# Kernel optimization log

Measured on AMD Instinct MI355X. Metric: run time of the kernel, lower is better.

The kernel has to match this reference:

```python
import jax, jax.numpy as jnp
import numpy as np

CROSS_SIZES = [256, 256, 256]  # split_half=True -> carried field sizes [39,128,128,256]


def setup_inputs() -> dict:
    key = jax.random.key(0)
    ks = jax.random.split(key, 6)
    B, F, D = 1024, 39, 32
    scale = 0.05
    return {
        "x": jax.random.normal(ks[0], (B, F, D), dtype=jnp.float32),
        "W0": jax.random.normal(ks[1], (F * F, 256), dtype=jnp.float32) * scale,
        "b0": jnp.zeros((256,), dtype=jnp.float32),
        "W1": jax.random.normal(ks[2], (F * 128, 256), dtype=jnp.float32) * scale,
        "b1": jnp.zeros((256,), dtype=jnp.float32),
        "W2": jax.random.normal(ks[3], (F * 128, 256), dtype=jnp.float32) * scale,
        "b2": jnp.zeros((256,), dtype=jnp.float32),
        "fc_w": jax.random.normal(ks[4], (512, 1), dtype=jnp.float32) * scale,
        "fc_b": jnp.zeros((1,), dtype=jnp.float32),
    }


def reference(x, W0, b0, W1, b1, W2, b2, fc_w, fc_b):
    # x: (B, F, D)
    B, F, D = x.shape
    params = [(W0, b0), (W1, b1), (W2, b2)]
    n_layers = len(params)
    x0 = x
    h = x            # carried state, (B, Hi, D)
    finals = []
    for i, (W, b) in enumerate(params):
        Hp = h.shape[1]
        # per-embedding-dim outer product of fields, flattened: (B, D, F*Hp)
        z = jnp.einsum('bfd,bhd->bdfh', x0, h).reshape(B, D, F * Hp)
        # conv1d with kernel width 1 == dense projection over the F*Hp axis
        out = jax.nn.relu(z @ W + b)          # (B, D, O)
        out = jnp.transpose(out, (0, 2, 1))   # (B, O, D)
        if i != n_layers - 1:
            half = CROSS_SIZES[i] // 2
            h = out[:, :half]        # next_tmp (first half)
            finals.append(out[:, half:])  # h (second half)
        else:
            finals.append(out)
    res = jnp.concatenate(finals, axis=1)  # (B, 512, D)
    res = jnp.sum(res, axis=-1)            # (B, 512)
    return res @ fc_w + fc_b               # (B, 1)
```

## Files before the change

kernel.cpp:

```cpp
#include <hip/hip_runtime.h>
#include <stdint.h>


typedef unsigned int u32;
typedef unsigned short u16;
typedef __attribute__((ext_vector_type(8))) unsigned short us8;
typedef __attribute__((ext_vector_type(8))) _Float16 half8;
typedef __attribute__((ext_vector_type(4))) float f32x4;

__device__ __forceinline__ u16 f32_to_f16u(float f) {
  union { _Float16 h; u16 u; } c;
  c.h = (_Float16)f;
  return c.u;
}
__device__ __forceinline__ u32 pkmul(u32 a, u32 b) {
  u32 r;
  asm("v_pk_mul_f16 %0, %1, %2" : "=v"(r) : "v"(a), "v"(b));
  return r;
}
__device__ __forceinline__ void gload16(const u16* g, u16* l) {
  __builtin_amdgcn_global_load_lds((const __attribute__((address_space(1))) u32*)g,
                                   (__attribute__((address_space(3))) u32*)l, 16, 0, 0);
}

__global__ void prep_wt(const float* __restrict__ W0, const float* __restrict__ W1,
                        const float* __restrict__ W2, u16* __restrict__ WT0,
                        u16* __restrict__ WT1, u16* __restrict__ WT2) {
  int blk = blockIdx.x;
  const float* W;
  u16* WT;
  int KPAD, kp0;
  bool l0 = false;
  if (blk < 312) { W = W0; WT = WT0; KPAD = 2496; kp0 = blk * 8; l0 = true; }
  else if (blk < 936) { W = W1; WT = WT1; KPAD = 4992; kp0 = (blk - 312) * 8; }
  else { W = W2; WT = WT2; KPAD = 4992; kp0 = (blk - 936) * 8; }

  __shared__ u16 lds[8][257];
  int t = threadIdx.x;
  #pragma unroll
  for (int kk = 0; kk < 8; ++kk) {
    int kp = kp0 + kk;
    float v;
    if (l0) {
      int f = kp >> 6, hh = kp & 63;
      v = (hh < 39) ? W[(f * 39 + hh) * 256 + t] : 0.f;
    } else {
      v = W[kp * 256 + t];
    }
    lds[kk][t] = f32_to_f16u(v);
  }
  __syncthreads();
  us8 o;
  #pragma unroll
  for (int kk = 0; kk < 8; ++kk) o[kk] = lds[kk][t];
  *(us8*)(&WT[(size_t)t * KPAD + kp0]) = o;
}

template <int LAYER>
__global__ __launch_bounds__(512, 2) void cin_layer(
    const float* __restrict__ x, const u16* __restrict__ hin,
    const u16* __restrict__ WT, const float* __restrict__ bias,
    u16* __restrict__ hout, float* __restrict__ fsum) {
  constexpr int HPAD = (LAYER == 0) ? 64 : 128;
  constexpr int HROW = HPAD + 8;
  constexpr int KPAD = 39 * HPAD;
  constexpr int HC2 = HPAD / 64;
  constexpr int NT = 39 * HC2;

  __shared__ __align__(16) u16 wtile[2][256 * 64];
  __shared__ __align__(16) u16 hT[4][32][HROW];
  __shared__ u32 x0pk[4][32][41];

  const int tid = threadIdx.x;
  const int bbase = blockIdx.x * 4;

  for (int idx = tid; idx < 4 * 1248; idx += 512) {
    int b = idx / 1248;
    int rem = idx - b * 1248;
    int f = rem >> 5, d = rem & 31;
    u16 xh = f32_to_f16u(x[(bbase + b) * 1248 + rem]);
    x0pk[b][d][f] = (u32)xh | ((u32)xh << 16);
    if (LAYER == 0) hT[b][d][f] = xh;
  }
  if (LAYER == 0) {
    for (int idx = tid; idx < 4 * 32 * 25; idx += 512) {
      int b = idx / 800;
      int rem = idx - b * 800;
      int d = rem / 25, p = rem - d * 25;
      hT[b][d][39 + p] = 0;
    }
  } else {
    for (int idx = tid; idx < 4 * 32 * 16; idx += 512) {
      int b = idx >> 9, rem = idx & 511;
      int d = rem >> 4, c = rem & 15;
      us8 v = *(const us8*)(&hin[(((bbase + b) * 32 + d) << 7) + c * 8]);
      *(us8*)(&hT[b][d][c * 8]) = v;
    }
  }

  const int lane = tid & 63;
  const int w = tid >> 6;
  const int l15 = lane & 15;
  const int g = lane >> 4;

  const int nloc = lane >> 3, slot = lane & 7;
  const int qq = slot ^ nloc;
  const int cp = qq >> 2, kcp = qq & 3;
  const u16* wsrc = WT + (size_t)(w * 32 + nloc) * KPAD + cp * 32 + kcp * 8;

  const int xorm = (l15 & 7) * 8;
  const int rB0 = (w * 32 + l15) * 64;

  f32x4 acc[8][2];
  #pragma unroll
  for (int m = 0; m < 8; ++m)
    #pragma unroll
    for (int n = 0; n < 2; ++n) acc[m][n] = (f32x4){0.f, 0.f, 0.f, 0.f};

  {
    u16* dst = &wtile[0][(w * 32) * 64];
    #pragma unroll
    for (int j = 0; j < 4; ++j) gload16(wsrc + (size_t)j * 8 * KPAD, dst + j * 8 * 64);
  }
  __syncthreads();

  union HF { u32 u[4]; half8 h; us8 s; };
  int tt = 0;
  for (int t = 0; t < HC2; ++t) {
    HF hf2[8][2];
    #pragma unroll
    for (int m = 0; m < 8; ++m)
      #pragma unroll
      for (int c = 0; c < 2; ++c)
        hf2[m][c].s = *(const us8*)(&hT[m >> 1][(m & 1) * 16 + l15][(2 * t + c) * 32 + g * 8]);
    for (int f = 0; f < 39; ++f, ++tt) {
      const int buf = tt & 1;
      if (tt + 1 < NT) {
        const int nf = (f + 1 < 39) ? f + 1 : 0;
        const int ntp = (f + 1 < 39) ? t : t + 1;
        const int koff = nf * HPAD + ntp * 64;
        u16* dst = &wtile[buf ^ 1][(w * 32) * 64];
        #pragma unroll
        for (int j = 0; j < 4; ++j)
          gload16(wsrc + (size_t)j * 8 * KPAD + koff, dst + j * 8 * 64);
      }
      u32 xs[8];
      #pragma unroll
      for (int m = 0; m < 8; ++m) xs[m] = x0pk[m >> 1][(m & 1) * 16 + l15][f];
      #pragma unroll
      for (int c = 0; c < 2; ++c) {
        const int off = (c * 32 + g * 8) ^ xorm;
        HF b0, b1;
        b0.s = *(const us8*)(&wtile[buf][rB0 + off]);
        b1.s = *(const us8*)(&wtile[buf][rB0 + 16 * 64 + off]);
        #pragma unroll
        for (int m = 0; m < 8; ++m) {
          HF a;
          #pragma unroll
          for (int i = 0; i < 4; ++i) a.u[i] = pkmul(hf2[m][c].u[i], xs[m]);
          acc[m][0] = __builtin_amdgcn_mfma_f32_16x16x32_f16(a.h, b0.h, acc[m][0], 0, 0, 0);
          acc[m][1] = __builtin_amdgcn_mfma_f32_16x16x32_f16(a.h, b1.h, acc[m][1], 0, 0, 0);
        }
      }
      __syncthreads();
    }
  }

  float bv[2];
  #pragma unroll
  for (int nt = 0; nt < 2; ++nt) bv[nt] = bias[w * 32 + nt * 16 + l15];

  if (LAYER < 2 && w < 4) {
    #pragma unroll
    for (int m = 0; m < 8; ++m)
      #pragma unroll
      for (int nt = 0; nt < 2; ++nt) {
        int o = w * 32 + nt * 16 + l15;
        #pragma unroll
        for (int r = 0; r < 4; ++r) {
          int row = m * 16 + g * 4 + r;
          int s = row >> 5, d = row & 31;
          float v = fmaxf(acc[m][nt][r] + bv[nt], 0.f);
          hout[(((bbase + s) * 32 + d) << 7) + o] = f32_to_f16u(v);
        }
      }
  } else {
    #pragma unroll
    for (int nt = 0; nt < 2; ++nt) {
      float sub[4] = {0.f, 0.f, 0.f, 0.f};
      #pragma unroll
      for (int m = 0; m < 8; ++m)
        #pragma unroll
        for (int r = 0; r < 4; ++r)
          sub[m >> 1] += fmaxf(acc[m][nt][r] + bv[nt], 0.f);
      #pragma unroll
      for (int s = 0; s < 4; ++s) {
        sub[s] += __shfl_xor(sub[s], 16);
        sub[s] += __shfl_xor(sub[s], 32);
      }
      if (lane < 16) {
        int o = w * 32 + nt * 16 + l15;
        int j = (LAYER == 0) ? (o - 128) : ((LAYER == 1) ? o : (256 + o));
        #pragma unroll
        for (int s = 0; s < 4; ++s) fsum[(bbase + s) * 512 + j] = sub[s];
      }
    }
  }
}

__global__ void finalize(const float* __restrict__ fsum, const float* __restrict__ fc_w,
                         const float* __restrict__ fc_b, float* __restrict__ out) {
  int b = blockIdx.x;
  int lane = threadIdx.x;
  const float* fs = fsum + (size_t)b * 512;
  float s = 0.f;
  #pragma unroll
  for (int k = 0; k < 8; ++k) {
    int j = k * 64 + lane;
    s += fs[j] * fc_w[j];
  }
  #pragma unroll
  for (int off = 32; off; off >>= 1) s += __shfl_xor(s, off);
  if (lane == 0) out[b] = s + fc_b[0];
}

extern "C" void kernel_launch(void* const* d_in, const int* in_sizes, int n_in,
                              void* d_out, int out_size, void* d_ws, size_t ws_size,
                              hipStream_t stream) {
  const float* x = (const float*)d_in[0];
  const float* W0 = (const float*)d_in[1];
  const float* b0 = (const float*)d_in[2];
  const float* W1 = (const float*)d_in[3];
  const float* b1 = (const float*)d_in[4];
  const float* W2 = (const float*)d_in[5];
  const float* b2 = (const float*)d_in[6];
  const float* fc_w = (const float*)d_in[7];
  const float* fc_b = (const float*)d_in[8];
  float* out = (float*)d_out;

  char* ws = (char*)d_ws;
  size_t oWT0 = 0;
  size_t oWT1 = oWT0 + (size_t)256 * 2496 * 2;
  size_t oWT2 = oWT1 + (size_t)256 * 4992 * 2;
  size_t oH = oWT2 + (size_t)256 * 4992 * 2;
  size_t oFS = oH + (size_t)1024 * 32 * 128 * 2;
  u16* WT0 = (u16*)(ws + oWT0);
  u16* WT1 = (u16*)(ws + oWT1);
  u16* WT2 = (u16*)(ws + oWT2);
  u16* hbuf = (u16*)(ws + oH);
  float* fsum = (float*)(ws + oFS);

  prep_wt<<<1560, 256, 0, stream>>>(W0, W1, W2, WT0, WT1, WT2);
  cin_layer<0><<<256, 512, 0, stream>>>(x, nullptr, WT0, b0, hbuf, fsum);
  cin_layer<1><<<256, 512, 0, stream>>>(x, hbuf, WT1, b1, hbuf, fsum);
  cin_layer<2><<<256, 512, 0, stream>>>(x, hbuf, WT2, b2, nullptr, fsum);
  finalize<<<1024, 64, 0, stream>>>(fsum, fc_w, fc_b, out);
}
```

Before: 235.7 us.

## Restructure CIN main loop with register prefetch and precomputed fp16 x0 layout

Adds a prep kernel that converts x0 into an fp16 layout ordered per d-lane/field, so each lane fetches its eight x0 scalars with one 16-byte global load instead of reading packed duplicates from LDS. Uses op_sel on v_pk_mul_f16 to broadcast the low or high half, which removes the duplicated packed x0 LDS array. The main loop is flattened and unrolled in pairs. Weight fragments for the next tile are read into registers after an explicit vmcnt wait instead of a per-tile __syncthreads. This is meant to cut LDS traffic and barrier stalls, but removing the block barrier while double-buffering through LDS risks races between waves, and the loop now carries more registers.

After: 196.8 us. -16.5%, faster.

```diff
diff --git a/kernel.cpp b/kernel.cpp
--- a/kernel.cpp
+++ b/kernel.cpp
@@ -13,14 +13,23 @@
   c.h = (_Float16)f;
   return c.u;
 }
-__device__ __forceinline__ u32 pkmul(u32 a, u32 b) {
+__device__ __forceinline__ u32 pkmul_blo(u32 a, u32 b) {
   u32 r;
-  asm("v_pk_mul_f16 %0, %1, %2" : "=v"(r) : "v"(a), "v"(b));
+  asm("v_pk_mul_f16 %0, %1, %2 op_sel:[0,0] op_sel_hi:[1,0]" : "=v"(r) : "v"(a), "v"(b));
+  return r;
+}
+__device__ __forceinline__ u32 pkmul_bhi(u32 a, u32 b) {
+  u32 r;
+  asm("v_pk_mul_f16 %0, %1, %2 op_sel:[0,1] op_sel_hi:[1,1]" : "=v"(r) : "v"(a), "v"(b));
   return r;
 }
 __device__ __forceinline__ void gload16(const u16* g, u16* l) {
   __builtin_amdgcn_global_load_lds((const __attribute__((address_space(1))) u32*)g,
                                    (__attribute__((address_space(3))) u32*)l, 16, 0, 0);
+}
+__device__ __forceinline__ void wait_vm0_sb() {
+  asm volatile("s_waitcnt vmcnt(0)" ::: "memory");
+  __builtin_amdgcn_sched_barrier(0);
 }
 
 __global__ void prep_wt(const float* __restrict__ W0, const float* __restrict__ W1,
@@ -56,11 +65,24 @@
   *(us8*)(&WT[(size_t)t * KPAD + kp0]) = o;
 }
 
+__global__ void prep_xg(const float* __restrict__ x, u16* __restrict__ xg) {
+  int bb = blockIdx.x;
+  int t = threadIdx.x;
+  for (int idx = t; idx < 4992; idx += 256) {
+    int dl = idx / 312;
+    int rem = idx - dl * 312;
+    int f = rem >> 3, m = rem & 7;
+    float v = x[(size_t)(bb * 4 + (m >> 1)) * 1248 + f * 32 + (m & 1) * 16 + dl];
+    xg[(size_t)bb * 4992 + idx] = f32_to_f16u(v);
+  }
+}
+
 template <int LAYER>
 __global__ __launch_bounds__(512, 2) void cin_layer(
     const float* __restrict__ x, const u16* __restrict__ hin,
-    const u16* __restrict__ WT, const float* __restrict__ bias,
-    u16* __restrict__ hout, float* __restrict__ fsum) {
+    const u16* __restrict__ WT, const u16* __restrict__ xg,
+    const float* __restrict__ bias, u16* __restrict__ hout,
+    float* __restrict__ fsum) {
   constexpr int HPAD = (LAYER == 0) ? 64 : 128;
   constexpr int HROW = HPAD + 8;
   constexpr int KPAD = 39 * HPAD;
@@ -69,20 +91,17 @@
 
   __shared__ __align__(16) u16 wtile[2][256 * 64];
   __shared__ __align__(16) u16 hT[4][32][HROW];
-  __shared__ u32 x0pk[4][32][41];
 
   const int tid = threadIdx.x;
   const int bbase = blockIdx.x * 4;
 
-  for (int idx = tid; idx < 4 * 1248; idx += 512) {
-    int b = idx / 1248;
-    int rem = idx - b * 1248;
-    int f = rem >> 5, d = rem & 31;
-    u16 xh = f32_to_f16u(x[(bbase + b) * 1248 + rem]);
-    x0pk[b][d][f] = (u32)xh | ((u32)xh << 16);
-    if (LAYER == 0) hT[b][d][f] = xh;
-  }
   if (LAYER == 0) {
+    for (int idx = tid; idx < 4 * 1248; idx += 512) {
+      int b = idx / 1248;
+      int rem = idx - b * 1248;
+      int f = rem >> 5, d = rem & 31;
+      hT[b][d][f] = f32_to_f16u(x[(bbase + b) * 1248 + rem]);
+    }
     for (int idx = tid; idx < 4 * 32 * 25; idx += 512) {
       int b = idx / 800;
       int rem = idx - b * 800;
@@ -105,11 +124,11 @@
 
   const int nloc = lane >> 3, slot = lane & 7;
   const int qq = slot ^ nloc;
-  const int cp = qq >> 2, kcp = qq & 3;
-  const u16* wsrc = WT + (size_t)(w * 32 + nloc) * KPAD + cp * 32 + kcp * 8;
+  const u16* wsrc = WT + (size_t)(w * 32 + nloc) * KPAD + qq * 8;
 
   const int xorm = (l15 & 7) * 8;
   const int rB0 = (w * 32 + l15) * 64;
+  const u16* xrow = xg + (size_t)blockIdx.x * 4992 + l15 * 312;
 
   f32x4 acc[8][2];
   #pragma unroll
@@ -125,46 +144,85 @@
   __syncthreads();
 
   union HF { u32 u[4]; half8 h; us8 s; };
-  int tt = 0;
-  for (int t = 0; t < HC2; ++t) {
-    HF hf2[8][2];
-    #pragma unroll
-    for (int m = 0; m < 8; ++m)
-      #pragma unroll
-      for (int c = 0; c < 2; ++c)
-        hf2[m][c].s = *(const us8*)(&hT[m >> 1][(m & 1) * 16 + l15][(2 * t + c) * 32 + g * 8]);
-    for (int f = 0; f < 39; ++f, ++tt) {
-      const int buf = tt & 1;
-      if (tt + 1 < NT) {
-        const int nf = (f + 1 < 39) ? f + 1 : 0;
-        const int ntp = (f + 1 < 39) ? t : t + 1;
-        const int koff = nf * HPAD + ntp * 64;
-        u16* dst = &wtile[buf ^ 1][(w * 32) * 64];
-        #pragma unroll
-        for (int j = 0; j < 4; ++j)
-          gload16(wsrc + (size_t)j * 8 * KPAD + koff, dst + j * 8 * 64);
-      }
-      u32 xs[8];
-      #pragma unroll
-      for (int m = 0; m < 8; ++m) xs[m] = x0pk[m >> 1][(m & 1) * 16 + l15][f];
-      #pragma unroll
-      for (int c = 0; c < 2; ++c) {
-        const int off = (c * 32 + g * 8) ^ xorm;
-        HF b0, b1;
-        b0.s = *(const us8*)(&wtile[buf][rB0 + off]);
-        b1.s = *(const us8*)(&wtile[buf][rB0 + 16 * 64 + off]);
-        #pragma unroll
-        for (int m = 0; m < 8; ++m) {
-          HF a;
-          #pragma unroll
-          for (int i = 0; i < 4; ++i) a.u[i] = pkmul(hf2[m][c].u[i], xs[m]);
-          acc[m][0] = __builtin_amdgcn_mfma_f32_16x16x32_f16(a.h, b0.h, acc[m][0], 0, 0, 0);
-          acc[m][1] = __builtin_amdgcn_mfma_f32_16x16x32_f16(a.h, b1.h, acc[m][1], 0, 0, 0);
-        }
-      }
-      __syncthreads();
-    }
-  }
+  union XQ { u32 u[4]; us8 s; };
+
+  HF hf2[8][2];
+  #pragma unroll
+  for (int m = 0; m < 8; ++m)
+    #pragma unroll
+    for (int c = 0; c < 2; ++c)
+      hf2[m][c].s = *(const us8*)(&hT[m >> 1][(m & 1) * 16 + l15][c * 32 + g * 8]);
+
+  HF fr[2][2];
+  XQ xqA, xqB;
+  #pragma unroll
+  for (int c = 0; c < 2; ++c) {
+    const int off = (c * 32 + g * 8) ^ xorm;
+    fr[c][0].s = *(const us8*)(&wtile[0][rB0 + off]);
+    fr[c][1].s = *(const us8*)(&wtile[0][rB0 + 16 * 64 + off]);
+  }
+  xqA.s = *(const us8*)(xrow);
+
+  int f = 0, hc = 0, tt = 0;
+
+#define TILE_BODY(XC, XN)                                                          \
+  {                                                                                \
+    const int buf = tt & 1;                                                        \
+    const bool more = (tt + 1 < NT);                                               \
+    int nf = f + 1, nhc = hc;                                                      \
+    if (nf == 39) { nf = 0; ++nhc; }                                               \
+    if (more) {                                                                    \
+      const int koff = nf * HPAD + nhc * 64;                                       \
+      u16* dst = &wtile[buf ^ 1][(w * 32) * 64];                                   \
+      _Pragma("unroll")                                                            \
+      for (int j = 0; j < 4; ++j)                                                  \
+        gload16(wsrc + (size_t)j * 8 * KPAD + koff, dst + j * 8 * 64);             \
+      XN.s = *(const us8*)(xrow + nf * 8);                                         \
+      __builtin_amdgcn_sched_barrier(0);                                           \
+    }                                                                              \
+    _Pragma("unroll")                                                              \
+    for (int c = 0; c < 2; ++c) {                                                  \
+      _Pragma("unroll")                                                            \
+      for (int m = 0; m < 8; ++m) {                                                \
+        HF a;                                                                      \
+        _Pragma("unroll")                                                          \
+        for (int i = 0; i < 4; ++i)                                                \
+          a.u[i] = (m & 1) ? pkmul_bhi(hf2[m][c].u[i], XC.u[m >> 1])               \
+                           : pkmul_blo(hf2[m][c].u[i], XC.u[m >> 1]);              \
+        acc[m][0] = __builtin_amdgcn_mfma_f32_16x16x32_f16(a.h, fr[c][0].h,        \
+                                                           acc[m][0], 0, 0, 0);    \
+        acc[m][1] = __builtin_amdgcn_mfma_f32_16x16x32_f16(a.h, fr[c][1].h,        \
+                                                           acc[m][1], 0, 0, 0);    \
+      }                                                                            \
+    }                                                                              \
+    if (more) {                                                                    \
+      wait_vm0_sb();                                                               \
+      _Pragma("unroll")                                                            \
+      for (int c = 0; c < 2; ++c) {                                                \
+        const int off = (c * 32 + g * 8) ^ xorm;                                   \
+        fr[c][0].s = *(const us8*)(&wtile[buf ^ 1][rB0 + off]);                    \
+        fr[c][1].s = *(const us8*)(&wtile[buf ^ 1][rB0 + 16 * 64 + off]);          \
+      }                                                                            \
+      if (nhc != hc) {                                                             \
+        _Pragma("unroll")                                                          \
+        for (int m = 0; m < 8; ++m)                                                \
+          _Pragma("unroll")                                                        \
+          for (int c = 0; c < 2; ++c)                                              \
+            hf2[m][c].s = *(const us8*)(                                           \
+                &hT[m >> 1][(m & 1) * 16 + l15][(2 * nhc + c) * 32 + g * 8]);      \
+      }                                                                            \
+    }                                                                              \
+    f = nf;                                                                        \
+    hc = nhc;                                                                      \
+    ++tt;                                                                          \
+  }
+
+  for (int p = 0; p < NT / 2; ++p) {
+    TILE_BODY(xqA, xqB);
+    TILE_BODY(xqB, xqA);
+  }
+  if (NT & 1) TILE_BODY(xqA, xqB);
+#undef TILE_BODY
 
   float bv[2];
   #pragma unroll
@@ -244,15 +302,18 @@
   size_t oWT2 = oWT1 + (size_t)256 * 4992 * 2;
   size_t oH = oWT2 + (size_t)256 * 4992 * 2;
   size_t oFS = oH + (size_t)1024 * 32 * 128 * 2;
+  size_t oXG = oFS + (size_t)1024 * 512 * 4;
   u16* WT0 = (u16*)(ws + oWT0);
   u16* WT1 = (u16*)(ws + oWT1);
   u16* WT2 = (u16*)(ws + oWT2);
   u16* hbuf = (u16*)(ws + oH);
   float* fsum = (float*)(ws + oFS);
+  u16* xg = (u16*)(ws + oXG);
 
   prep_wt<<<1560, 256, 0, stream>>>(W0, W1, W2, WT0, WT1, WT2);
-  cin_layer<0><<<256, 512, 0, stream>>>(x, nullptr, WT0, b0, hbuf, fsum);
-  cin_layer<1><<<256, 512, 0, stream>>>(x, hbuf, WT1, b1, hbuf, fsum);
-  cin_layer<2><<<256, 512, 0, stream>>>(x, hbuf, WT2, b2, nullptr, fsum);
+  prep_xg<<<256, 256, 0, stream>>>(x, xg);
+  cin_layer<0><<<256, 512, 0, stream>>>(x, nullptr, WT0, xg, b0, hbuf, fsum);
+  cin_layer<1><<<256, 512, 0, stream>>>(x, hbuf, WT1, xg, b1, hbuf, fsum);
+  cin_layer<2><<<256, 512, 0, stream>>>(x, hbuf, WT2, xg, b2, nullptr, fsum);
   finalize<<<1024, 64, 0, stream>>>(fsum, fc_w, fc_b, out);
 }
```
